# Performance work log

Measured on AMD Instinct MI355X. Metric: run time of the kernel, lower is better.

## Reference

```python
import jax, jax.numpy as jnp
import numpy as np

EPS = 1e-5


def setup_inputs() -> dict:
    key = jax.random.key(0)
    k1, k2, k3 = jax.random.split(key, 3)
    B, n_per, C_in, C_out = 8, 131072, 32, 64
    N = B * n_per
    coord = jax.random.uniform(k1, (N, 3), dtype=jnp.float32)          # points in unit cube
    feat = jax.random.normal(k2, (N, C_in), dtype=jnp.float32)
    offset = (jnp.arange(1, B + 1, dtype=jnp.int32) * n_per)           # cumulative counts
    W = jax.random.normal(k3, (C_in, C_out), dtype=jnp.float32) * 0.05  # fc weight (no bias)
    gamma = jnp.ones((C_out,), dtype=jnp.float32)
    beta = jnp.zeros((C_out,), dtype=jnp.float32)
    return {"coord": coord, "feat": feat, "offset": offset, "W": W,
            "gamma": gamma, "beta": beta, "grid_size": 0.05}


def reference(coord, feat, offset, W, gamma, beta, grid_size):
    N = coord.shape[0]
    B = offset.shape[0]
    # offset2batch: point i belongs to batch = first b with i < offset[b]
    batch = jnp.searchsorted(offset, jnp.arange(N, dtype=offset.dtype), side="right").astype(jnp.int32)

    # fc -> BatchNorm (training-mode batch stats, biased var) -> ReLU
    h = feat @ W                                                        # [N, C_out]
    mean = h.mean(axis=0)
    var = jnp.mean((h - mean) ** 2, axis=0)
    h = jax.nn.relu((h - mean) * jax.lax.rsqrt(var + EPS) * gamma + beta)

    # start = per-batch min coord (segment_csr 'min' over batch pointer)
    start = jax.ops.segment_min(coord, batch, num_segments=B)           # [B, 3]

    # voxel_grid: integer voxel coords per point, combined with batch into a unique key
    v = jnp.floor((coord - start[batch]) / grid_size).astype(jnp.int32)  # [N, 3] >= 0
    D = v.max(axis=0) + 1                                               # grid extents
    vkey = ((batch * D[0] + v[:, 0]) * D[1] + v[:, 1]) * D[2] + v[:, 2]

    # unique(sorted) + inverse + counts; then segment mean/max by cluster
    uniq, inverse, counts = jnp.unique(vkey, return_inverse=True, return_counts=True)
    inverse = inverse.reshape(-1).astype(jnp.int32)
    M = uniq.shape[0]
    coord_out = jax.ops.segment_sum(coord, inverse, num_segments=M) / counts[:, None].astype(coord.dtype)
    feat_out = jax.ops.segment_max(h, inverse, num_segments=M)

    # batch id of each cluster (constant within cluster) -> new offset
    batch_out = jax.ops.segment_min(batch, inverse, num_segments=M)
    offset_out = jnp.cumsum(jnp.bincount(batch_out, length=B)).astype(offset.dtype)
    return coord_out, feat_out, offset_out, inverse
```

## Files before the change

kernel.cpp:

```cpp
#include <hip/hip_runtime.h>
#include <float.h>

#define EPSV 1e-5f
#define DGRID 21
#define DPROD (21 * 21 * 21)

typedef __attribute__((ext_vector_type(8))) short bf16x8;
typedef __attribute__((ext_vector_type(4))) float f32x4;

__device__ __forceinline__ short f2bf(float x) {
    unsigned u = __float_as_uint(x);
    unsigned r = (u + 0x7FFFu + ((u >> 16) & 1u)) >> 16;
    return (short)r;
}

__device__ __forceinline__ int batch_of(int i, const int* __restrict__ offset, int B) {
    int b = 0;
    while (b < B - 1 && i >= offset[b]) ++b;
    return b;
}

__global__ void k_init(int* startEnc, int B) {
    int tid = threadIdx.x;
    if (tid < B * 3) startEnc[tid] = 0x7FFFFFFF;
}

__global__ void k_start(const float* __restrict__ coord, const int* __restrict__ offset,
                        int* startEnc, int* counts, int KSM, int N, int B) {
    int gtid = blockIdx.x * blockDim.x + threadIdx.x;
    for (int k = gtid; k < KSM; k += gridDim.x * blockDim.x) counts[k] = 0;

    __shared__ int smin[24];
    int t = threadIdx.x;
    if (t < B * 3) smin[t] = 0x7FFFFFFF;
    __syncthreads();
    int base = gtid * 4;
    int curb = -1;
    int m0 = 0x7FFFFFFF, m1 = 0x7FFFFFFF, m2 = 0x7FFFFFFF;
    for (int r = 0; r < 4; ++r) {
        int i = base + r;
        if (i >= N) break;
        int b = batch_of(i, offset, B);
        if (b != curb) {
            if (curb >= 0) {
                atomicMin(&smin[curb * 3 + 0], m0);
                atomicMin(&smin[curb * 3 + 1], m1);
                atomicMin(&smin[curb * 3 + 2], m2);
            }
            curb = b; m0 = m1 = m2 = 0x7FFFFFFF;
        }
        m0 = min(m0, __float_as_int(coord[(size_t)i * 3 + 0]));
        m1 = min(m1, __float_as_int(coord[(size_t)i * 3 + 1]));
        m2 = min(m2, __float_as_int(coord[(size_t)i * 3 + 2]));
    }
    if (curb >= 0) {
        atomicMin(&smin[curb * 3 + 0], m0);
        atomicMin(&smin[curb * 3 + 1], m1);
        atomicMin(&smin[curb * 3 + 2], m2);
    }
    __syncthreads();
    if (t < B * 3 && smin[t] != 0x7FFFFFFF) atomicMin(&startEnc[t], smin[t]);
}

__global__ void k_count(const float* __restrict__ coord, const int* __restrict__ offset,
                        const int* __restrict__ startEnc, const float* __restrict__ gsP,
                        int* counts, int* vkey, int N, int B) {
    int i = blockIdx.x * blockDim.x + threadIdx.x;
    if (i >= N) return;
    float inv_gs = 1.0f / gsP[0];
    int b = batch_of(i, offset, B);
    float s0 = __int_as_float(startEnc[b * 3 + 0]);
    float s1 = __int_as_float(startEnc[b * 3 + 1]);
    float s2 = __int_as_float(startEnc[b * 3 + 2]);
    int vx = min(DGRID - 1, (int)floorf((coord[(size_t)i * 3 + 0] - s0) * inv_gs));
    int vy = min(DGRID - 1, (int)floorf((coord[(size_t)i * 3 + 1] - s1) * inv_gs));
    int vz = min(DGRID - 1, (int)floorf((coord[(size_t)i * 3 + 2] - s2) * inv_gs));
    int k = ((b * DGRID + vx) * DGRID + vy) * DGRID + vz;
    vkey[i] = k;
    atomicAdd(&counts[k], 1);
}

__global__ void k_scan1(const int* __restrict__ counts, int* occPart, int* cntPart, int KSM) {
    __shared__ int so[256], sc[256];
    int t = threadIdx.x;
    int base = blockIdx.x * 1024 + t * 4;
    int o = 0, c = 0;
    for (int r = 0; r < 4; ++r) {
        int k = base + r;
        if (k < KSM) { int cnt = counts[k]; o += (cnt > 0); c += cnt; }
    }
    so[t] = o; sc[t] = c;
    __syncthreads();
    for (int s = 128; s > 0; s >>= 1) {
        if (t < s) { so[t] += so[t + s]; sc[t] += sc[t + s]; }
        __syncthreads();
    }
    if (t == 0) { occPart[blockIdx.x] = so[0]; cntPart[blockIdx.x] = sc[0]; }
}

__global__ void k_scan2(const int* occPart, const int* cntPart,
                        int* occPartEx, int* cntPartEx, int NBLK) {
    __shared__ int so[128], sc[128];
    int t = threadIdx.x;
    int o = (t < NBLK) ? occPart[t] : 0;
    int c = (t < NBLK) ? cntPart[t] : 0;
    so[t] = o; sc[t] = c;
    __syncthreads();
    for (int s = 1; s < 128; s <<= 1) {
        int ao = 0, ac = 0;
        if (t >= s) { ao = so[t - s]; ac = sc[t - s]; }
        __syncthreads();
        so[t] += ao; sc[t] += ac;
        __syncthreads();
    }
    if (t < NBLK) { occPartEx[t] = so[t] - o; cntPartEx[t] = sc[t] - c; }
}

__global__ void k_scan3(const int* __restrict__ counts, const int* occPartEx, const int* cntPartEx,
                        int* occScan, int* cntScan, int* cursor, int* cntC, int* cstartC, int KSM) {
    __shared__ int so[256], sc[256];
    int t = threadIdx.x;
    int base = blockIdx.x * 1024 + t * 4;
    int o[4], c[4];
    int tO = 0, tC = 0;
    for (int r = 0; r < 4; ++r) {
        int k = base + r;
        int cnt = (k < KSM) ? counts[k] : 0;
        o[r] = (cnt > 0); c[r] = cnt;
        tO += o[r]; tC += c[r];
    }
    so[t] = tO; sc[t] = tC;
    __syncthreads();
    for (int s = 1; s < 256; s <<= 1) {
        int ao = 0, ac = 0;
        if (t >= s) { ao = so[t - s]; ac = sc[t - s]; }
        __syncthreads();
        so[t] += ao; sc[t] += ac;
        __syncthreads();
    }
    int exO = so[t] - tO + occPartEx[blockIdx.x];
    int exC = sc[t] - tC + cntPartEx[blockIdx.x];
    for (int r = 0; r < 4; ++r) {
        int k = base + r;
        if (k < KSM) {
            occScan[k] = exO; cntScan[k] = exC; cursor[k] = 0;
            if (c[r] > 0) { cntC[exO] = c[r]; cstartC[exO] = exC; }
            exO += o[r]; exC += c[r];
        }
    }
}

__global__ void k_scatter(const int* __restrict__ vkey,
                          const int* __restrict__ occScan, const int* __restrict__ cntScan,
                          int* cursor,
                          const float* __restrict__ feat, const float* __restrict__ coord,
                          short* __restrict__ featR, float* __restrict__ coordR,
                          float* __restrict__ dout, int N, int B, int M) {
    int i = blockIdx.x * blockDim.x + threadIdx.x;
    if (i >= N) return;
    int k = vkey[i];
    int cidx = occScan[k];
    int pos = cntScan[k] + atomicAdd(&cursor[k], 1);
    dout[(size_t)67 * M + B + i] = (float)cidx;

    const float4* fp = reinterpret_cast<const float4*>(feat + (size_t)i * 32);
    bf16x8* dst = reinterpret_cast<bf16x8*>(featR + (size_t)pos * 32);
#pragma unroll
    for (int t = 0; t < 4; ++t) {
        float4 a = fp[2 * t];
        float4 b2 = fp[2 * t + 1];
        bf16x8 r;
        r[0] = f2bf(a.x);  r[1] = f2bf(a.y);  r[2] = f2bf(a.z);  r[3] = f2bf(a.w);
        r[4] = f2bf(b2.x); r[5] = f2bf(b2.y); r[6] = f2bf(b2.z); r[7] = f2bf(b2.w);
        dst[t] = r;
    }
    float4 cv;
    cv.x = coord[(size_t)i * 3 + 0];
    cv.y = coord[(size_t)i * 3 + 1];
    cv.z = coord[(size_t)i * 3 + 2];
    cv.w = 0.f;
    *reinterpret_cast<float4*>(coordR + (size_t)pos * 4) = cv;
}

__launch_bounds__(64)
__global__ void k_pool(const short* __restrict__ featR, const float* __restrict__ coordR,
                       const float* __restrict__ W,
                       const int* __restrict__ cstartC, const int* __restrict__ cntC,
                       float* __restrict__ dout, float* __restrict__ statPart, int M) {
    const int lane = threadIdx.x;
    const int col  = lane & 15;
    const int quad = lane >> 4;
    const int nw = gridDim.x;
    const int gw = blockIdx.x;

    bf16x8 Bf[4];
#pragma unroll
    for (int t = 0; t < 4; ++t) {
#pragma unroll
        for (int j = 0; j < 8; ++j) {
            int k = quad * 8 + j;
            Bf[t][j] = f2bf(W[k * 64 + t * 16 + col]);
        }
    }

    float sumA[4] = {0.f, 0.f, 0.f, 0.f};
    float sqA[4]  = {0.f, 0.f, 0.f, 0.f};

    for (int c0 = 2 * gw; c0 < M; c0 += 2 * nw) {
        int c1 = c0 + 1;
        bool has2 = (c1 < M);
        if (!has2) c1 = c0;
        int ps0 = cstartC[c0], n0 = cntC[c0];
        int ps1 = cstartC[c1], n1 = cntC[c1];
        int nmax = max(n0, n1);

        float maxA0[4] = {-FLT_MAX, -FLT_MAX, -FLT_MAX, -FLT_MAX};
        float maxA1[4] = {-FLT_MAX, -FLT_MAX, -FLT_MAX, -FLT_MAX};
        float cacc0 = 0.f, cacc1 = 0.f;

        for (int base = 0; base < nmax; base += 16) {
            int m = base + col;
            int idx0 = min(m, n0 - 1);
            int idx1 = min(m, n1 - 1);
            bf16x8 Af0 = *reinterpret_cast<const bf16x8*>(featR + (size_t)(ps0 + idx0) * 32 + quad * 8);
            bf16x8 Af1 = *reinterpret_cast<const bf16x8*>(featR + (size_t)(ps1 + idx1) * 32 + quad * 8);
            if (quad > 0) {
                float v0 = coordR[(size_t)(ps0 + idx0) * 4 + (quad - 1)];
                float v1 = coordR[(size_t)(ps1 + idx1) * 4 + (quad - 1)];
                cacc0 += (m < n0) ? v0 : 0.f;
                cacc1 += (m < n1) ? v1 : 0.f;
            }
            f32x4 Cz = {0.f, 0.f, 0.f, 0.f};
#pragma unroll
            for (int t = 0; t < 4; ++t) {
                f32x4 v0 = __builtin_amdgcn_mfma_f32_16x16x32_bf16(Af0, Bf[t], Cz, 0, 0, 0);
                f32x4 v1 = __builtin_amdgcn_mfma_f32_16x16x32_bf16(Af1, Bf[t], Cz, 0, 0, 0);
#pragma unroll
                for (int r = 0; r < 4; ++r) {
                    int rowPt = base + quad * 4 + r;
                    maxA0[t] = fmaxf(maxA0[t], v0[r]);
                    maxA1[t] = fmaxf(maxA1[t], v1[r]);
                    float m0 = (rowPt < n0) ? v0[r] : 0.f;
                    sumA[t] += m0; sqA[t] = fmaf(m0, m0, sqA[t]);
                    float m1 = (rowPt < n1 && has2) ? v1[r] : 0.f;
                    sumA[t] += m1; sqA[t] = fmaf(m1, m1, sqA[t]);
                }
            }
        }
        float out0 = 0.f, out1 = 0.f;
#pragma unroll
        for (int t = 0; t < 4; ++t) {
            float v = maxA0[t];
            v = fmaxf(v, __shfl_xor(v, 16, 64));
            v = fmaxf(v, __shfl_xor(v, 32, 64));
            if (quad == t) out0 = v;
            float w = maxA1[t];
            w = fmaxf(w, __shfl_xor(w, 16, 64));
            w = fmaxf(w, __shfl_xor(w, 32, 64));
            if (quad == t) out1 = w;
        }
        dout[(size_t)3 * M + (size_t)c0 * 64 + lane] = out0;
        dout[(size_t)3 * M + (size_t)c1 * 64 + lane] = out1;

        cacc0 += __shfl_xor(cacc0, 1, 64); cacc0 += __shfl_xor(cacc0, 2, 64);
        cacc0 += __shfl_xor(cacc0, 4, 64); cacc0 += __shfl_xor(cacc0, 8, 64);
        cacc1 += __shfl_xor(cacc1, 1, 64); cacc1 += __shfl_xor(cacc1, 2, 64);
        cacc1 += __shfl_xor(cacc1, 4, 64); cacc1 += __shfl_xor(cacc1, 8, 64);
        if (quad > 0 && col == 0) {
            dout[(size_t)c0 * 3 + (quad - 1)] = cacc0 / (float)n0;
            dout[(size_t)c1 * 3 + (quad - 1)] = cacc1 / (float)n1;
        }
    }

    float so = 0.f, qo = 0.f;
#pragma unroll
    for (int t = 0; t < 4; ++t) {
        float s = sumA[t];
        s += __shfl_xor(s, 16, 64);
        s += __shfl_xor(s, 32, 64);
        float q = sqA[t];
        q += __shfl_xor(q, 16, 64);
        q += __shfl_xor(q, 32, 64);
        if (quad == t) { so = s; qo = q; }
    }
    statPart[(size_t)gw * 128 + lane] = so;
    statPart[(size_t)gw * 128 + 64 + lane] = qo;
}

__global__ void k_statred(const float* __restrict__ statPart,
                          const float* __restrict__ gamma, const float* __restrict__ beta,
                          float* bnA, float* bnB, int NB, int N) {
    __shared__ float s1[256], s2[256];
    int c = blockIdx.x;
    int t = threadIdx.x;
    float a = 0.f, b = 0.f;
    for (int bb = t; bb < NB; bb += 256) {
        a += statPart[(size_t)bb * 128 + c];
        b += statPart[(size_t)bb * 128 + 64 + c];
    }
    s1[t] = a; s2[t] = b;
    __syncthreads();
    for (int s = 128; s > 0; s >>= 1) {
        if (t < s) { s1[t] += s1[t + s]; s2[t] += s2[t + s]; }
        __syncthreads();
    }
    if (t == 0) {
        float invN = 1.0f / (float)N;
        float mean = s1[0] * invN;
        float var = s2[0] * invN - mean * mean;
        float aa = gamma[c] / sqrtf(var + EPSV);
        bnA[c] = aa;
        bnB[c] = beta[c] - mean * aa;
    }
}

__global__ void k_final(float* __restrict__ dout, const float* __restrict__ bnA,
                        const float* __restrict__ bnB,
                        const int* __restrict__ occScan, int M, int B) {
    size_t stride = (size_t)gridDim.x * blockDim.x;
    size_t tid0 = (size_t)blockIdx.x * blockDim.x + threadIdx.x;
    size_t totF = (size_t)M * 64;
    for (size_t t = tid0; t < totF; t += stride) {
        int c = (int)(t & 63);
        float v = dout[(size_t)3 * M + t];
        dout[(size_t)3 * M + t] = fmaxf(bnA[c] * v + bnB[c], 0.f);
    }
    if (tid0 < (size_t)B) {
        int val = (tid0 == (size_t)(B - 1)) ? M : occScan[(int)(tid0 + 1) * DPROD];
        dout[(size_t)67 * M + tid0] = (float)val;
    }
}

extern "C" void kernel_launch(void* const* d_in, const int* in_sizes, int n_in,
                              void* d_out, int out_size, void* d_ws, size_t ws_size,
                              hipStream_t stream) {
    const float* coord = (const float*)d_in[0];
    const float* feat  = (const float*)d_in[1];
    const int*   offset = (const int*)d_in[2];
    const float* W     = (const float*)d_in[3];
    const float* gamma = (const float*)d_in[4];
    const float* beta  = (const float*)d_in[5];
    const float* gsP   = (const float*)d_in[6];
    float* dout = (float*)d_out;

    const int N = in_sizes[0] / 3;
    const int B = in_sizes[2];
    const int M = (out_size - B - N) / 67;
    const int KSM = B * DPROD;
    const int NBLK = (KSM + 1023) / 1024;
    const int NBPL = 8192;

    int* wsI = (int*)d_ws;
    int* startEnc  = wsI + 0;
    float* bnA     = (float*)(wsI + 64);
    float* bnB     = (float*)(wsI + 128);
    int* occPart   = wsI + 256;
    int* cntPart   = wsI + 384;
    int* occPartEx = wsI + 512;
    int* cntPartEx = wsI + 640;
    int* counts    = wsI + 1024;
    int* occScan   = counts + KSM;
    int* cntScan   = occScan + KSM;
    int* cursor    = cntScan + KSM;
    int* cntC      = cursor + KSM;
    int* cstartC   = cntC + KSM;
    int* vkey      = cstartC + KSM;
    float* statPart = (float*)(vkey + N);
    short* featR   = (short*)(statPart + (size_t)NBPL * 128);
    float* coordR  = (float*)(featR + (size_t)N * 32);

    const int TPB = 256;
    int gChunk = (N + 1023) / 1024;
    int gPoint = (N + TPB - 1) / TPB;

    k_init<<<1, 64, 0, stream>>>(startEnc, B);
    k_start<<<gChunk, TPB, 0, stream>>>(coord, offset, startEnc, counts, KSM, N, B);
    k_count<<<gPoint, TPB, 0, stream>>>(coord, offset, startEnc, gsP, counts, vkey, N, B);
    k_scan1<<<NBLK, TPB, 0, stream>>>(counts, occPart, cntPart, KSM);
    k_scan2<<<1, 128, 0, stream>>>(occPart, cntPart, occPartEx, cntPartEx, NBLK);
    k_scan3<<<NBLK, TPB, 0, stream>>>(counts, occPartEx, cntPartEx, occScan, cntScan,
                                      cursor, cntC, cstartC, KSM);
    k_scatter<<<gPoint, TPB, 0, stream>>>(vkey, occScan, cntScan, cursor,
                                          feat, coord, featR, coordR, dout, N, B, M);
    k_pool<<<NBPL, 64, 0, stream>>>(featR, coordR, W, cstartC, cntC, dout, statPart, M);
    k_statred<<<64, 256, 0, stream>>>(statPart, gamma, beta, bnA, bnB, NBPL, N);
    k_final<<<1024, TPB, 0, stream>>>(dout, bnA, bnB, occScan, M, B);
}
```

Measured before the change: 393.0 us.

## Split scatter into position pass and gather-based materialization with packed key records

```diff
diff --git a/kernel.cpp b/kernel.cpp
--- a/kernel.cpp
+++ b/kernel.cpp
@@ -117,7 +117,7 @@
 }
 
 __global__ void k_scan3(const int* __restrict__ counts, const int* occPartEx, const int* cntPartEx,
-                        int* occScan, int* cntScan, int* cursor, int* cntC, int* cstartC, int KSM) {
+                        int4* krec, int* cntC, int* cstartC, int KSM) {
     __shared__ int so[256], sc[256];
     int t = threadIdx.x;
     int base = blockIdx.x * 1024 + t * 4;
@@ -143,26 +143,31 @@
     for (int r = 0; r < 4; ++r) {
         int k = base + r;
         if (k < KSM) {
-            occScan[k] = exO; cntScan[k] = exC; cursor[k] = 0;
+            krec[k] = make_int4(exO, exC, 0, 0);
             if (c[r] > 0) { cntC[exO] = c[r]; cstartC[exO] = exC; }
             exO += o[r]; exC += c[r];
         }
     }
 }
 
-__global__ void k_scatter(const int* __restrict__ vkey,
-                          const int* __restrict__ occScan, const int* __restrict__ cntScan,
-                          int* cursor,
-                          const float* __restrict__ feat, const float* __restrict__ coord,
-                          short* __restrict__ featR, float* __restrict__ coordR,
-                          float* __restrict__ dout, int N, int B, int M) {
+__global__ void k_pos(const int* __restrict__ vkey, int4* __restrict__ krec,
+                      int* __restrict__ plist, float* __restrict__ dout,
+                      int N, int B, int M) {
     int i = blockIdx.x * blockDim.x + threadIdx.x;
     if (i >= N) return;
     int k = vkey[i];
-    int cidx = occScan[k];
-    int pos = cntScan[k] + atomicAdd(&cursor[k], 1);
-    dout[(size_t)67 * M + B + i] = (float)cidx;
-
+    int4 rec = krec[k];
+    int pos = rec.y + atomicAdd(&(((int*)krec)[(size_t)4 * k + 2]), 1);
+    plist[pos] = i;
+    dout[(size_t)67 * M + B + i] = (float)rec.x;
+}
+
+__global__ void k_mat(const int* __restrict__ plist,
+                      const float* __restrict__ feat, const float* __restrict__ coord,
+                      short* __restrict__ featR, float* __restrict__ coordR, int N) {
+    int pos = blockIdx.x * blockDim.x + threadIdx.x;
+    if (pos >= N) return;
+    int i = plist[pos];
     const float4* fp = reinterpret_cast<const float4*>(feat + (size_t)i * 32);
     bf16x8* dst = reinterpret_cast<bf16x8*>(featR + (size_t)pos * 32);
 #pragma unroll
@@ -316,7 +321,7 @@
 
 __global__ void k_final(float* __restrict__ dout, const float* __restrict__ bnA,
                         const float* __restrict__ bnB,
-                        const int* __restrict__ occScan, int M, int B) {
+                        const int4* __restrict__ krec, int M, int B) {
     size_t stride = (size_t)gridDim.x * blockDim.x;
     size_t tid0 = (size_t)blockIdx.x * blockDim.x + threadIdx.x;
     size_t totF = (size_t)M * 64;
@@ -326,7 +331,7 @@
         dout[(size_t)3 * M + t] = fmaxf(bnA[c] * v + bnB[c], 0.f);
     }
     if (tid0 < (size_t)B) {
-        int val = (tid0 == (size_t)(B - 1)) ? M : occScan[(int)(tid0 + 1) * DPROD];
+        int val = (tid0 == (size_t)(B - 1)) ? M : krec[(size_t)(tid0 + 1) * DPROD].x;
         dout[(size_t)67 * M + tid0] = (float)val;
     }
 }
@@ -359,13 +364,12 @@
     int* occPartEx = wsI + 512;
     int* cntPartEx = wsI + 640;
     int* counts    = wsI + 1024;
-    int* occScan   = counts + KSM;
-    int* cntScan   = occScan + KSM;
-    int* cursor    = cntScan + KSM;
-    int* cntC      = cursor + KSM;
+    int4* krec     = (int4*)(counts + KSM);
+    int* cntC      = (int*)(krec + KSM);
     int* cstartC   = cntC + KSM;
     int* vkey      = cstartC + KSM;
-    float* statPart = (float*)(vkey + N);
+    int* plist     = vkey + N;
+    float* statPart = (float*)(plist + N);
     short* featR   = (short*)(statPart + (size_t)NBPL * 128);
     float* coordR  = (float*)(featR + (size_t)N * 32);
 
@@ -378,11 +382,10 @@
     k_count<<<gPoint, TPB, 0, stream>>>(coord, offset, startEnc, gsP, counts, vkey, N, B);
     k_scan1<<<NBLK, TPB, 0, stream>>>(counts, occPart, cntPart, KSM);
     k_scan2<<<1, 128, 0, stream>>>(occPart, cntPart, occPartEx, cntPartEx, NBLK);
-    k_scan3<<<NBLK, TPB, 0, stream>>>(counts, occPartEx, cntPartEx, occScan, cntScan,
-                                      cursor, cntC, cstartC, KSM);
-    k_scatter<<<gPoint, TPB, 0, stream>>>(vkey, occScan, cntScan, cursor,
-                                          feat, coord, featR, coordR, dout, N, B, M);
+    k_scan3<<<NBLK, TPB, 0, stream>>>(counts, occPartEx, cntPartEx, krec, cntC, cstartC, KSM);
+    k_pos<<<gPoint, TPB, 0, stream>>>(vkey, krec, plist, dout, N, B, M);
+    k_mat<<<gPoint, TPB, 0, stream>>>(plist, feat, coord, featR, coordR, N);
     k_pool<<<NBPL, 64, 0, stream>>>(featR, coordR, W, cstartC, cntC, dout, statPart, M);
     k_statred<<<64, 256, 0, stream>>>(statPart, gamma, beta, bnA, bnB, NBPL, N);
-    k_final<<<1024, TPB, 0, stream>>>(dout, bnA, bnB, occScan, M, B);
-}
+    k_final<<<1024, TPB, 0, stream>>>(dout, bnA, bnB, krec, M, B);
+}
```

Measured after the change: 461.2 us. +17.4%, slower.
